# Kernel tuning notes

Measured on AMD Instinct MI355X. Metric: run time of the kernel, lower is better.

The kernel has to match this reference:

```python
import jax, jax.numpy as jnp
import numpy as np

N = 50000   # nodes
E = 800000  # edges (avg degree 16)
IN = 128
HID = 128
OUT = 64    # num classes


def setup_inputs() -> dict:
    key = jax.random.key(0)
    ks = jax.random.split(key, 10)
    x = jax.random.normal(ks[0], (N, IN), dtype=jnp.float32)
    edge_src = jax.random.randint(ks[1], (E,), 0, N)
    edge_dst = jax.random.randint(ks[2], (E,), 0, N)
    y = jax.random.randint(ks[3], (N,), 0, OUT)
    train_mask = jax.random.bernoulli(ks[4], 0.5, (N,))
    w = lambda k, sh: (jax.random.normal(k, sh, dtype=jnp.float32) * (1.0 / np.sqrt(sh[0]))).astype(jnp.float32)
    return dict(
        x=x, edge_src=edge_src, edge_dst=edge_dst, y=y, train_mask=train_mask,
        W1l=w(ks[5], (IN, HID)), b1=jnp.zeros((HID,), jnp.float32), W1r=w(ks[6], (IN, HID)),
        W2l=w(ks[7], (HID, OUT)), b2=jnp.zeros((OUT,), jnp.float32), W2r=w(ks[8], (HID, OUT)),
    )


def mean_aggr(h, src, dst, n):
    # sparse adjacency matmul with reduce='mean': for each dst node, mean of src features
    msg_sum = jax.ops.segment_sum(h[src], dst, num_segments=n)          # [N, D]
    cnt = jax.ops.segment_sum(jnp.ones((src.shape[0],), h.dtype), dst, num_segments=n)
    return msg_sum / jnp.maximum(cnt, 1.0)[:, None]


def reference(x, edge_src, edge_dst, y, train_mask, W1l, b1, W1r, W2l, b2, W2r):
    n = x.shape[0]
    # dropout(p=0.2, training=False) is identity in eval mode
    h = x
    # layer 1: SAGEConv = lin_l(mean_aggr(h)) + lin_r(h), then ReLU (+identity dropout)
    a = mean_aggr(h, edge_src, edge_dst, n)
    h = jax.nn.relu(a @ W1l + b1 + h @ W1r)
    # layer 2 (output layer)
    a = mean_aggr(h, edge_src, edge_dst, n)
    logits = a @ W2l + b2 + h @ W2r
    logp = jax.nn.log_softmax(logits, axis=1)
    # nll_loss over masked nodes (single chunk => loss / num_chunks with num_chunks=1)
    m = train_mask.astype(logp.dtype)
    nll = -jnp.take_along_axis(logp, y[:, None], axis=1)[:, 0]
    loss = jnp.sum(nll * m) / jnp.maximum(jnp.sum(m), 1.0)
    return loss
```

## Files before the change

kernel.cpp:

```cpp
#include <hip/hip_runtime.h>
#include <hip/hip_bf16.h>

typedef unsigned int uint;
typedef unsigned short u16;

#define DIN 128
#define DHID 128
#define DOUT 64
#define BSH 8
#define P3CHUNK 8192
#define P4MAX 6144

static inline size_t al256(size_t x) { return (x + 255) & ~(size_t)255; }

typedef __attribute__((ext_vector_type(8))) short short8;
typedef __attribute__((ext_vector_type(4))) float floatx4;
typedef __attribute__((ext_vector_type(2))) float floatx2;
typedef __attribute__((ext_vector_type(4))) int intx4;

__device__ inline float2 bf2x(uint v) {
    return make_float2(__uint_as_float(v << 16), __uint_as_float(v & 0xffff0000u));
}
__device__ inline uint packbf(float a, float b) {
    uint ua = __float_as_uint(a), ub = __float_as_uint(b);
    ua += 0x7fff + ((ua >> 16) & 1);
    ub += 0x7fff + ((ub >> 16) & 1);
    return (ua >> 16) | (ub & 0xffff0000u);
}
__device__ inline u16 pb(float a) {
    uint u = __float_as_uint(a);
    u += 0x7fff + ((u >> 16) & 1);
    return (u16)(u >> 16);
}

__device__ inline floatx2 f8lo(uint v) {
#if __has_builtin(__builtin_amdgcn_cvt_pk_f32_fp8)
    return __builtin_amdgcn_cvt_pk_f32_fp8((int)v, false);
#else
    uint b0 = v & 0xffu, b1 = (v >> 8) & 0xffu;
    floatx2 r;
    r.x = __uint_as_float(((b0 & 0x80u) << 24) | ((b0 & 0x7fu) << 20)) * 0x1p120f;
    r.y = __uint_as_float(((b1 & 0x80u) << 24) | ((b1 & 0x7fu) << 20)) * 0x1p120f;
    return r;
#endif
}
__device__ inline floatx2 f8hi(uint v) {
#if __has_builtin(__builtin_amdgcn_cvt_pk_f32_fp8)
    return __builtin_amdgcn_cvt_pk_f32_fp8((int)v, true);
#else
    uint b0 = (v >> 16) & 0xffu, b1 = (v >> 24) & 0xffu;
    floatx2 r;
    r.x = __uint_as_float(((b0 & 0x80u) << 24) | ((b0 & 0x7fu) << 20)) * 0x1p120f;
    r.y = __uint_as_float(((b1 & 0x80u) << 24) | ((b1 & 0x7fu) << 20)) * 0x1p120f;
    return r;
#endif
}
__device__ inline uint enc8(float f) {
    uint ub = __float_as_uint(f * 0x1p-120f);
    uint s = (ub >> 24) & 0x80u;
    uint mag = ub & 0x7fffffffu;
    mag += 0x7ffffu + ((mag >> 20) & 1u);
    uint r = mag >> 20;
    if (r > 0x7eu) r = 0x7eu;
    return r | s;
}
__device__ inline uint packf8x4(float a, float b, float c, float d) {
#if __has_builtin(__builtin_amdgcn_cvt_pk_fp8_f32)
    int p = __builtin_amdgcn_cvt_pk_fp8_f32(a, b, 0, false);
    p = __builtin_amdgcn_cvt_pk_fp8_f32(c, d, p, true);
    return (uint)p;
#else
    return enc8(a) | (enc8(b) << 8) | (enc8(c) << 16) | (enc8(d) << 24);
#endif
}

__global__ __launch_bounds__(256) void pack_detect_kernel(
    const float* __restrict__ W1l, const float* __restrict__ W1r,
    const float* __restrict__ W2l, const float* __restrict__ W2r,
    u16* __restrict__ Wp1, u16* __restrict__ Wp2,
    const int* __restrict__ tm, int n_int, int* __restrict__ gflags) {
    if (blockIdx.x < 192) {
        int id = blockIdx.x * 256 + threadIdx.x;
        if (id < 32768) {
            int frag = id >> 9, e = id & 511;
            int lane = e >> 3, j = e & 7;
            int kc = frag >> 4, tn = frag & 15;
            int k = kc * 32 + (lane >> 4) * 8 + j;
            int ncol = tn * 16 + (lane & 15);
            float v = (ncol < 128) ? W1l[k * 128 + ncol] : W1r[k * 128 + ncol - 128];
            Wp1[id] = pb(v);
        } else if (id < 49152) {
            int id2 = id - 32768;
            int frag = id2 >> 9, e = id2 & 511;
            int lane = e >> 3, j = e & 7;
            int kc = frag >> 3, tn = frag & 7;
            int k = kc * 32 + (lane >> 4) * 8 + j;
            int ncol = tn * 16 + (lane & 15);
            float v = (ncol < 64) ? W2l[k * 64 + ncol] : W2r[k * 64 + ncol - 64];
            Wp2[id2] = pb(v);
        }
    } else {
        int i = (blockIdx.x - 192) * 256 + threadIdx.x;
        bool hf = false, ho = false;
        for (; i < n_int; i += 64 * 256) {
            int v = tm[i];
            hf |= (v == 0x3F800000);
            ho |= (v != 0 && v != 1 && v != 0x3F800000);
        }
        if (__any(hf) && (threadIdx.x & 63) == 0) atomicOr(&gflags[0], 1);
        if (__any(ho) && (threadIdx.x & 63) == 0) atomicOr(&gflags[1], 1);
    }
}

__global__ __launch_bounds__(256) void bhist_kernel(const int* __restrict__ dst, int e, int nb,
                                                    uint* __restrict__ bcounts) {
    __shared__ uint lh[512];
    for (int i = threadIdx.x; i < 512; i += 256) lh[i] = 0;
    __syncthreads();
    int nquad = (e + 3) >> 2;
    for (int i = blockIdx.x * 256 + threadIdx.x; i < nquad; i += gridDim.x * 256) {
        int base = i * 4;
        if (base + 4 <= e) {
            intx4 d = __builtin_nontemporal_load((const intx4*)(dst + base));
            atomicAdd(&lh[d.x >> BSH], 1u);
            atomicAdd(&lh[d.y >> BSH], 1u);
            atomicAdd(&lh[d.z >> BSH], 1u);
            atomicAdd(&lh[d.w >> BSH], 1u);
        } else {
            for (int k = base; k < e; ++k) atomicAdd(&lh[dst[k] >> BSH], 1u);
        }
    }
    __syncthreads();
    for (int i = threadIdx.x; i < nb; i += 256) {
        uint c = lh[i];
        if (c) atomicAdd(&bcounts[i], c);
    }
}

__global__ __launch_bounds__(256) void bscan_kernel(const uint* __restrict__ bcounts, int nb, int e,
                                                    uint* __restrict__ bbase, uint* __restrict__ bcursor,
                                                    int* __restrict__ offsets, int n) {
    __shared__ uint pws[4];
    int t = threadIdx.x;
    uint v0 = (2 * t < nb) ? bcounts[2 * t] : 0u;
    uint v1 = (2 * t + 1 < nb) ? bcounts[2 * t + 1] : 0u;
    uint s = v0 + v1;
    int lane = t & 63, wv = t >> 6;
    uint incl = s;
    #pragma unroll
    for (int d = 1; d < 64; d <<= 1) {
        uint u = (uint)__shfl_up((int)incl, d, 64);
        if (lane >= d) incl += u;
    }
    if (lane == 63) pws[wv] = incl;
    __syncthreads();
    uint woff = 0;
    #pragma unroll
    for (int i = 0; i < 4; ++i) if (i < wv) woff += pws[i];
    uint excl = woff + incl - s;
    if (2 * t < nb) { bbase[2 * t] = excl; bcursor[2 * t] = excl; }
    if (2 * t + 1 < nb) { bbase[2 * t + 1] = excl + v0; bcursor[2 * t + 1] = excl + v0; }
    if (t == 0) {
        uint tot = pws[0] + pws[1] + pws[2] + pws[3];
        bbase[nb] = tot;
        offsets[n] = e;
    }
}

__global__ __launch_bounds__(256) void partition_kernel(const int* __restrict__ src,
                                                        const int* __restrict__ dst, int e, int nb,
                                                        uint* __restrict__ bcursor,
                                                        uint* __restrict__ pairs) {
    __shared__ uint lh[512], lexcl[512], lbase[512], lpos[512];
    __shared__ uint st[P3CHUNK];
    __shared__ uint pws[4];
    int t = threadIdx.x;
    int e0 = blockIdx.x * P3CHUNK;
    int ecnt = min(P3CHUNK, e - e0);
    for (int i = t; i < 512; i += 256) { lh[i] = 0; lpos[i] = 0; }
    __syncthreads();
    for (int i = t; i < ecnt; i += 256)
        atomicAdd(&lh[dst[e0 + i] >> BSH], 1u);
    __syncthreads();
    {
        uint v0 = lh[2 * t], v1 = lh[2 * t + 1];
        uint s = v0 + v1;
        int lane = t & 63, wv = t >> 6;
        uint incl = s;
        #pragma unroll
        for (int d = 1; d < 64; d <<= 1) {
            uint u = (uint)__shfl_up((int)incl, d, 64);
            if (lane >= d) incl += u;
        }
        if (lane == 63) pws[wv] = incl;
        __syncthreads();
        uint woff = 0;
        #pragma unroll
        for (int i = 0; i < 4; ++i) if (i < wv) woff += pws[i];
        uint excl = woff + incl - s;
        lexcl[2 * t] = excl;
        lexcl[2 * t + 1] = excl + v0;
    }
    __syncthreads();
    for (int b = t; b < nb; b += 256) {
        uint c = lh[b];
        lbase[b] = c ? atomicAdd(&bcursor[b], c) : 0u;
    }
    __syncthreads();
    for (int i = t; i < ecnt; i += 256) {
        int d = dst[e0 + i];
        int s = src[e0 + i];
        int b = d >> BSH;
        uint slot = lexcl[b] + atomicAdd(&lpos[b], 1u);
        st[slot] = ((uint)(d & ((1 << BSH) - 1)) << 16) | (uint)s;
    }
    __syncthreads();
    int wv = t >> 6, lane = t & 63;
    for (int b = wv; b < nb; b += 4) {
        uint c = lh[b];
        uint lsrc = lexcl[b], gdst = lbase[b];
        for (uint k = lane; k < c; k += 64)
            pairs[gdst + k] = st[lsrc + k];
    }
}

__global__ __launch_bounds__(256) void emit_kernel(const uint* __restrict__ pairs,
                                                   const uint* __restrict__ bbase, int n,
                                                   u16* __restrict__ csr, int* __restrict__ offsets) {
    __shared__ uint cnt[256], lex[256];
    __shared__ u16 ob[P4MAX];
    __shared__ uint pws[4];
    int b = blockIdx.x, t = threadIdx.x;
    uint seg0 = bbase[b];
    int len = (int)(bbase[b + 1] - seg0);
    int n0 = b << BSH;
    cnt[t] = 0;
    __syncthreads();
    for (int i = t; i < len; i += 256)
        atomicAdd(&cnt[pairs[seg0 + i] >> 16], 1u);
    __syncthreads();
    uint v = cnt[t];
    int lane = t & 63, wv = t >> 6;
    uint incl = v;
    #pragma unroll
    for (int d = 1; d < 64; d <<= 1) {
        uint u = (uint)__shfl_up((int)incl, d, 64);
        if (lane >= d) incl += u;
    }
    if (lane == 63) pws[wv] = incl;
    __syncthreads();
    uint woff = 0;
    #pragma unroll
    for (int i = 0; i < 4; ++i) if (i < wv) woff += pws[i];
    uint excl = woff + incl - v;
    lex[t] = excl;
    if (n0 + t < n) offsets[n0 + t] = (int)(seg0 + excl);
    __syncthreads();
    cnt[t] = 0;
    __syncthreads();
    for (int i = t; i < len; i += 256) {
        uint p = pairs[seg0 + i];
        uint loc = p >> 16;
        uint slot = lex[loc] + atomicAdd(&cnt[loc], 1u);
        if (slot < P4MAX) ob[slot] = (u16)(p & 0xffffu);
        else csr[seg0 + slot] = (u16)(p & 0xffffu);
    }
    __syncthreads();
    int lim = min(len, P4MAX);
    for (int i = t; i < lim; i += 256) csr[seg0 + i] = ob[i];
}

__global__ __launch_bounds__(256) void hist_kernel(const int* __restrict__ dst, int e,
                                                   int* __restrict__ counts) {
    int base = (blockIdx.x * 256 + threadIdx.x) * 4;
    if (base + 4 <= e) {
        intx4 d = __builtin_nontemporal_load((const intx4*)(dst + base));
        atomicAdd(&counts[d.x], 1);
        atomicAdd(&counts[d.y], 1);
        atomicAdd(&counts[d.z], 1);
        atomicAdd(&counts[d.w], 1);
    } else {
        for (int i = base; i < e; ++i) atomicAdd(&counts[dst[i]], 1);
    }
}

__global__ __launch_bounds__(256) void scan_partial_kernel(const int* __restrict__ counts, int n,
                                                           int* __restrict__ partials) {
    int t = threadIdx.x;
    int base = blockIdx.x * 1024 + t * 4;
    int s = 0;
    if (base + 3 < n) {
        int4 v = *(const int4*)&counts[base];
        s = v.x + v.y + v.z + v.w;
    } else {
        for (int i = 0; i < 4; ++i) if (base + i < n) s += counts[base + i];
    }
    #pragma unroll
    for (int d = 32; d; d >>= 1) s += __shfl_down(s, d, 64);
    __shared__ int wsum[4];
    if ((t & 63) == 0) wsum[t >> 6] = s;
    __syncthreads();
    if (t == 0) partials[blockIdx.x] = wsum[0] + wsum[1] + wsum[2] + wsum[3];
}

__global__ void scan_top_kernel(int* __restrict__ partials, int nparts, int* __restrict__ total_out) {
    int lane = threadIdx.x;
    int v = (lane < nparts) ? partials[lane] : 0;
    int incl = v;
    #pragma unroll
    for (int d = 1; d < 64; d <<= 1) {
        int u = __shfl_up(incl, d, 64);
        if (lane >= d) incl += u;
    }
    if (lane < nparts) partials[lane] = incl - v;
    if (lane == 63) *total_out = incl;
}

__global__ __launch_bounds__(256) void scan_final_kernel(const int* __restrict__ counts, int n,
                                                         const int* __restrict__ partials,
                                                         int* __restrict__ offsets,
                                                         int* __restrict__ cursor) {
    int t = threadIdx.x;
    int base = blockIdx.x * 1024 + t * 4;
    int v0 = 0, v1 = 0, v2 = 0, v3 = 0;
    if (base + 3 < n) {
        int4 q = *(const int4*)&counts[base];
        v0 = q.x; v1 = q.y; v2 = q.z; v3 = q.w;
    } else {
        if (base + 0 < n) v0 = counts[base + 0];
        if (base + 1 < n) v1 = counts[base + 1];
        if (base + 2 < n) v2 = counts[base + 2];
        if (base + 3 < n) v3 = counts[base + 3];
    }
    int s = v0 + v1 + v2 + v3;
    int lane = t & 63, wid = t >> 6;
    int incl = s;
    #pragma unroll
    for (int d = 1; d < 64; d <<= 1) {
        int u = __shfl_up(incl, d, 64);
        if (lane >= d) incl += u;
    }
    __shared__ int wsum[4];
    if (lane == 63) wsum[wid] = incl;
    __syncthreads();
    int woff = 0;
    #pragma unroll
    for (int i = 0; i < 4; ++i) if (i < wid) woff += wsum[i];
    int run = partials[blockIdx.x] + woff + incl - s;
    if (base + 0 < n) { offsets[base + 0] = run; cursor[base + 0] = run; run += v0; }
    if (base + 1 < n) { offsets[base + 1] = run; cursor[base + 1] = run; run += v1; }
    if (base + 2 < n) { offsets[base + 2] = run; cursor[base + 2] = run; run += v2; }
    if (base + 3 < n) { offsets[base + 3] = run; cursor[base + 3] = run; run += v3; }
}

__global__ __launch_bounds__(256) void scatter_kernel(const int* __restrict__ src,
                                                      const int* __restrict__ dst, int e,
                                                      int* __restrict__ cursor,
                                                      uint* __restrict__ csr_src) {
    int base = (blockIdx.x * 256 + threadIdx.x) * 4;
    if (base + 4 <= e) {
        intx4 s = __builtin_nontemporal_load((const intx4*)(src + base));
        intx4 d = __builtin_nontemporal_load((const intx4*)(dst + base));
        int p0 = atomicAdd(&cursor[d.x], 1);
        int p1 = atomicAdd(&cursor[d.y], 1);
        int p2 = atomicAdd(&cursor[d.z], 1);
        int p3 = atomicAdd(&cursor[d.w], 1);
        csr_src[p0] = (uint)s.x;
        csr_src[p1] = (uint)s.y;
        csr_src[p2] = (uint)s.z;
        csr_src[p3] = (uint)s.w;
    } else {
        for (int i = base; i < e; ++i) {
            int p = atomicAdd(&cursor[dst[i]], 1);
            csr_src[p] = (uint)src[i];
        }
    }
}

__global__ __launch_bounds__(256) void gemm1_mfma(
    const float* __restrict__ X, const u16* __restrict__ Wp1,
    const float* __restrict__ b1,
    uint* __restrict__ P1f8, uint* __restrict__ Q1u, int n) {
    __shared__ u16 ep[4][16][260];
    int t = threadIdx.x;
    int w = t >> 6, lane = t & 63;
    int q = lane >> 4, c = lane & 15;
    int m0 = blockIdx.x * 64 + w * 16;
    int me = min(m0 + c, n - 1);
    const float* xrow = X + (size_t)me * 128 + q * 8;
    const u16* wbase = Wp1 + lane * 8;

    floatx4 acc[16];
    #pragma unroll
    for (int i = 0; i < 16; ++i) acc[i] = (floatx4){0.f, 0.f, 0.f, 0.f};

    #pragma unroll
    for (int kc = 0; kc < 4; ++kc) {
        float4 x0 = *(const float4*)(xrow + kc * 32);
        float4 x1 = *(const float4*)(xrow + kc * 32 + 4);
        union { short8 s; uint4 u; } a;
        a.u.x = packbf(x0.x, x0.y); a.u.y = packbf(x0.z, x0.w);
        a.u.z = packbf(x1.x, x1.y); a.u.w = packbf(x1.z, x1.w);
        #pragma unroll
        for (int tn = 0; tn < 16; ++tn) {
            union { short8 s; uint4 u; } b;
            b.u = *(const uint4*)(wbase + (kc * 16 + tn) * 512);
            acc[tn] = __builtin_amdgcn_mfma_f32_16x16x32_bf16(a.s, b.s, acc[tn], 0, 0, 0);
        }
    }

    #pragma unroll
    for (int tn = 0; tn < 16; ++tn) {
        int col = tn * 16 + c;
        float badd = (tn >= 8) ? b1[col - 128] : 0.f;
        #pragma unroll
        for (int i = 0; i < 4; ++i)
            ep[w][q * 4 + i][col] = pb(acc[tn][i] + badd);
    }
    for (int r = 0; r < 16; ++r) {
        int grow = m0 + r;
        if (grow >= n) break;
        uint2 v = *(const uint2*)&ep[w][r][lane * 4];
        if (lane < 32) {
            float2 e0 = bf2x(v.x), e1 = bf2x(v.y);
            P1f8[(size_t)grow * 32 + lane] = packf8x4(e0.x, e0.y, e1.x, e1.y);
        } else {
            *(uint2*)&Q1u[(size_t)grow * 64 + 2 * (lane - 32)] = v;
        }
    }
}

template <typename IT>
__global__ __launch_bounds__(256) void aggr1_kernel(
    const uint* __restrict__ P1f8, const uint* __restrict__ Q1u,
    const int* __restrict__ offsets, const IT* __restrict__ csr,
    uint* __restrict__ h1u, int n) {
    int node = (int)((blockIdx.x * (size_t)blockDim.x + threadIdx.x) >> 6);
    int lane = threadIdx.x & 63;
    int l = lane & 31, hw = lane >> 5;
    if (node >= n) return;
    int beg = offsets[node], end = offsets[node + 1];
    float a0 = 0.f, a1 = 0.f, a2 = 0.f, a3 = 0.f;
    int i = beg + hw;
    for (; i + 2 < end; i += 4) {
        int s0 = csr[i], s1 = csr[i + 2];
        uint v0 = P1f8[(size_t)s0 * 32 + l];
        uint v1 = P1f8[(size_t)s1 * 32 + l];
        floatx2 u0 = f8lo(v0), w0 = f8hi(v0);
        floatx2 u1 = f8lo(v1), w1 = f8hi(v1);
        a0 += u0.x + u1.x; a1 += u0.y + u1.y;
        a2 += w0.x + w1.x; a3 += w0.y + w1.y;
    }
    for (; i < end; i += 2) {
        int s = csr[i];
        uint v = P1f8[(size_t)s * 32 + l];
        floatx2 u = f8lo(v), w2 = f8hi(v);
        a0 += u.x; a1 += u.y; a2 += w2.x; a3 += w2.y;
    }
    a0 += __shfl_xor(a0, 32, 64);
    a1 += __shfl_xor(a1, 32, 64);
    a2 += __shfl_xor(a2, 32, 64);
    a3 += __shfl_xor(a3, 32, 64);
    if (hw == 0) {
        float inv = 1.0f / (float)max(end - beg, 1);
        uint2 qv = *(const uint2*)&Q1u[(size_t)node * 64 + l * 2];
        float2 q0 = bf2x(qv.x), q1 = bf2x(qv.y);
        float r0 = fmaxf(fmaf(a0, inv, q0.x), 0.f);
        float r1 = fmaxf(fmaf(a1, inv, q0.y), 0.f);
        float r2 = fmaxf(fmaf(a2, inv, q1.x), 0.f);
        float r3 = fmaxf(fmaf(a3, inv, q1.y), 0.f);
        uint2 o;
        o.x = packbf(r0, r1);
        o.y = packbf(r2, r3);
        *(uint2*)&h1u[(size_t)node * 64 + l * 2] = o;
    }
}

__global__ __launch_bounds__(256) void gemm2_mfma(
    const uint* __restrict__ H1u, const u16* __restrict__ Wp2,
    const float* __restrict__ b2,
    uint* __restrict__ P2f8, uint* __restrict__ Q2u, int n) {
    __shared__ u16 ep[4][16][132];
    int t = threadIdx.x;
    int w = t >> 6, lane = t & 63;
    int q = lane >> 4, c = lane & 15;
    int m0 = blockIdx.x * 64 + w * 16;
    int me = min(m0 + c, n - 1);
    const u16* hrow = (const u16*)H1u + (size_t)me * 128 + q * 8;
    const u16* wbase = Wp2 + lane * 8;

    floatx4 acc[8];
    #pragma unroll
    for (int i = 0; i < 8; ++i) acc[i] = (floatx4){0.f, 0.f, 0.f, 0.f};

    #pragma unroll
    for (int kc = 0; kc < 4; ++kc) {
        union { short8 s; uint4 u; } a;
        a.u = *(const uint4*)(hrow + kc * 32);
        #pragma unroll
        for (int tn = 0; tn < 8; ++tn) {
            union { short8 s; uint4 u; } b;
            b.u = *(const uint4*)(wbase + (kc * 8 + tn) * 512);
            acc[tn] = __builtin_amdgcn_mfma_f32_16x16x32_bf16(a.s, b.s, acc[tn], 0, 0, 0);
        }
    }

    #pragma unroll
    for (int tn = 0; tn < 8; ++tn) {
        int col = tn * 16 + c;
        float badd = (tn >= 4) ? b2[col - 64] : 0.f;
        #pragma unroll
        for (int i = 0; i < 4; ++i)
            ep[w][q * 4 + i][col] = pb(acc[tn][i] + badd);
    }
    for (int r = 0; r < 16; ++r) {
        int grow = m0 + r;
        if (grow >= n) break;
        if (lane < 16) {
            uint2 v = *(const uint2*)&ep[w][r][lane * 4];
            float2 e0 = bf2x(v.x), e1 = bf2x(v.y);
            P2f8[(size_t)grow * 16 + lane] = packf8x4(e0.x, e0.y, e1.x, e1.y);
        } else if (lane < 48) {
            uint v = *(const uint*)&ep[w][r][64 + (lane - 16) * 2];
            Q2u[(size_t)grow * 32 + (lane - 16)] = v;
        }
    }
}

template <typename IT>
__global__ __launch_bounds__(1024) void loss_kernel(
    const uint* __restrict__ P2f8, const uint* __restrict__ Q2u,
    const int* __restrict__ offsets, const IT* __restrict__ csr,
    const int* __restrict__ y, const void* __restrict__ tmask,
    const int* __restrict__ gflags, float2* __restrict__ bpart, int n) {
    int wid = threadIdx.x >> 6;
    int node = blockIdx.x * 16 + wid;
    int lane = threadIdx.x & 63;
    int l = lane & 15, qw = lane >> 4;
    float num = 0.f, den = 0.f;
    if (node < n) {
        int beg = offsets[node], end = offsets[node + 1];
        float a0 = 0.f, a1 = 0.f, a2 = 0.f, a3 = 0.f;
        int i = beg + qw;
        for (; i + 4 < end; i += 8) {
            int s0 = csr[i], s1 = csr[i + 4];
            uint v0 = P2f8[(size_t)s0 * 16 + l];
            uint v1 = P2f8[(size_t)s1 * 16 + l];
            floatx2 u0 = f8lo(v0), w0 = f8hi(v0);
            floatx2 u1 = f8lo(v1), w1 = f8hi(v1);
            a0 += u0.x + u1.x; a1 += u0.y + u1.y;
            a2 += w0.x + w1.x; a3 += w0.y + w1.y;
        }
        for (; i < end; i += 4) {
            int s = csr[i];
            uint v = P2f8[(size_t)s * 16 + l];
            floatx2 u = f8lo(v), w2 = f8hi(v);
            a0 += u.x; a1 += u.y; a2 += w2.x; a3 += w2.y;
        }
        #pragma unroll
        for (int d = 16; d <= 32; d <<= 1) {
            a0 += __shfl_xor(a0, d, 64);
            a1 += __shfl_xor(a1, d, 64);
            a2 += __shfl_xor(a2, d, 64);
            a3 += __shfl_xor(a3, d, 64);
        }
        float inv = 1.0f / (float)max(end - beg, 1);
        uint2 qv = *(const uint2*)&Q2u[(size_t)node * 32 + l * 2];
        float2 q0 = bf2x(qv.x), q1 = bf2x(qv.y);
        float L0 = fmaf(a0, inv, q0.x);
        float L1 = fmaf(a1, inv, q0.y);
        float L2 = fmaf(a2, inv, q1.x);
        float L3 = fmaf(a3, inv, q1.y);
        float mx = fmaxf(fmaxf(L0, L1), fmaxf(L2, L3));
        #pragma unroll
        for (int d = 1; d <= 8; d <<= 1) mx = fmaxf(mx, __shfl_xor(mx, d, 64));
        float s = __expf(L0 - mx) + __expf(L1 - mx) + __expf(L2 - mx) + __expf(L3 - mx);
        #pragma unroll
        for (int d = 1; d <= 8; d <<= 1) s += __shfl_xor(s, d, 64);
        int cls = y[node];
        int srcl = (cls >> 2) & 15;
        float c0 = __shfl(L0, srcl, 64);
        float c1 = __shfl(L1, srcl, 64);
        float c2 = __shfl(L2, srcl, 64);
        float c3 = __shfl(L3, srcl, 64);
        int sel = cls & 3;
        float Lc = (sel == 0) ? c0 : (sel == 1) ? c1 : (sel == 2) ? c2 : c3;
        float logp = (Lc - mx) - __logf(s);
        int f = gflags[0] ? 2 : (gflags[1] ? 0 : 1);
        bool m;
        if (f == 0)      m = ((const unsigned char*)tmask)[node] != 0;
        else if (f == 1) m = ((const int*)tmask)[node] != 0;
        else             m = ((const float*)tmask)[node] != 0.f;
        if (m) { num = -logp; den = 1.f; }
    }
    __shared__ float2 wacc[16];
    if (lane == 0) wacc[wid] = make_float2(num, den);
    __syncthreads();
    if (threadIdx.x == 0) {
        float rx = 0.f, ry = 0.f;
        #pragma unroll
        for (int i = 0; i < 16; ++i) { rx += wacc[i].x; ry += wacc[i].y; }
        bpart[blockIdx.x] = make_float2(rx, ry);
    }
}

__global__ __launch_bounds__(1024) void finalize_kernel(const float2* __restrict__ bpart, int nb,
                                                        float* __restrict__ out) {
    int t = threadIdx.x;
    float sx = 0.f, sy = 0.f;
    for (int i = t; i < nb; i += 1024) { float2 v = bpart[i]; sx += v.x; sy += v.y; }
    #pragma unroll
    for (int d = 32; d; d >>= 1) { sx += __shfl_down(sx, d, 64); sy += __shfl_down(sy, d, 64); }
    __shared__ float2 wacc[16];
    if ((t & 63) == 0) wacc[t >> 6] = make_float2(sx, sy);
    __syncthreads();
    if (t == 0) {
        float nx = 0.f, ny = 0.f;
        #pragma unroll
        for (int i = 0; i < 16; ++i) { nx += wacc[i].x; ny += wacc[i].y; }
        out[0] = nx / fmaxf(ny, 1.f);
    }
}

extern "C" void kernel_launch(void* const* d_in, const int* in_sizes, int n_in,
                              void* d_out, int out_size, void* d_ws, size_t ws_size,
                              hipStream_t stream) {
    const float* x        = (const float*)d_in[0];
    const int*   edge_src = (const int*)d_in[1];
    const int*   edge_dst = (const int*)d_in[2];
    const int*   y        = (const int*)d_in[3];
    const void*  tmask    = (const void*)d_in[4];
    const float* W1l      = (const float*)d_in[5];
    const float* b1       = (const float*)d_in[6];
    const float* W1r      = (const float*)d_in[7];
    const float* W2l      = (const float*)d_in[8];
    const float* b2       = (const float*)d_in[9];
    const float* W2r      = (const float*)d_in[10];

    const int N = in_sizes[0] / DIN;
    const int E = in_sizes[1];
    const int nb_loss = (N + 15) / 16;
    const bool small_idx = (N <= 65535);
    const int nb = (N + 255) >> BSH;

    char* ws = (char*)d_ws;
    int* gflags = (int*)ws;
    size_t off = 256;
    int* offsets  = (int*)(ws + off); off += al256(((size_t)N + 1) * 4);
    uint* bcounts = (uint*)(ws + off); off += al256(513 * 4);
    uint* bbase   = (uint*)(ws + off); off += al256(513 * 4);
    uint* bcursor = (uint*)(ws + off); off += al256(513 * 4);
    uint* pairs   = (uint*)(ws + off); off += al256((size_t)E * 4);
    void* csr     = (void*)(ws + off); off += al256((size_t)E * 4);
    int* counts   = (int*)(ws + off); off += al256((size_t)N * 4);
    int* cursor   = (int*)(ws + off); off += al256((size_t)N * 4);
    int* spart    = (int*)(ws + off); off += al256(64 * 4);
    float2* bpart = (float2*)(ws + off); off += al256((size_t)nb_loss * 8);
    u16* Wp1      = (u16*)(ws + off); off += al256(32768 * 2);
    u16* Wp2      = (u16*)(ws + off); off += al256(16384 * 2);
    uint* P1f8    = (uint*)(ws + off); off += al256((size_t)N * 32 * 4);
    uint* h1u     = (uint*)(ws + off); off += al256((size_t)N * 64 * 4);
    uint* Q1u     = (uint*)(ws + off); off += al256((size_t)N * 64 * 4);
    uint* P2f8    = Q1u;
    uint* Q2u     = Q1u + (size_t)N * 16;

    hipMemsetAsync(ws, 0, 256, stream);

    pack_detect_kernel<<<256, 256, 0, stream>>>(W1l, W1r, W2l, W2r, Wp1, Wp2,
                                                (const int*)tmask, N / 4, gflags);

    if (small_idx) {
        hipMemsetAsync(bcounts, 0, 513 * 4, stream);
        bhist_kernel<<<256, 256, 0, stream>>>(edge_dst, E, nb, bcounts);
        bscan_kernel<<<1, 256, 0, stream>>>(bcounts, nb, E, bbase, bcursor, offsets, N);
        int pblocks = (E + P3CHUNK - 1) / P3CHUNK;
        partition_kernel<<<pblocks, 256, 0, stream>>>(edge_src, edge_dst, E, nb, bcursor, pairs);
        emit_kernel<<<nb, 256, 0, stream>>>(pairs, bbase, N, (u16*)csr, offsets);
    } else {
        hipMemsetAsync(counts, 0, (size_t)N * 4, stream);
        int eb4 = (E + 1023) / 1024;
        hist_kernel<<<eb4, 256, 0, stream>>>(edge_dst, E, counts);
        int sb = (N + 1023) / 1024;
        scan_partial_kernel<<<sb, 256, 0, stream>>>(counts, N, spart);
        scan_top_kernel<<<1, 64, 0, stream>>>(spart, sb, &offsets[N]);
        scan_final_kernel<<<sb, 256, 0, stream>>>(counts, N, spart, offsets, cursor);
        scatter_kernel<<<eb4, 256, 0, stream>>>(edge_src, edge_dst, E, cursor, (uint*)csr);
    }

    int gb = (N + 63) / 64;
    int ab = (N + 3) / 4;

    gemm1_mfma<<<gb, 256, 0, stream>>>(x, Wp1, b1, P1f8, Q1u, N);
    if (small_idx)
        aggr1_kernel<u16><<<ab, 256, 0, stream>>>(P1f8, Q1u, offsets, (const u16*)csr, h1u, N);
    else
        aggr1_kernel<uint><<<ab, 256, 0, stream>>>(P1f8, Q1u, offsets, (const uint*)csr, h1u, N);
    gemm2_mfma<<<gb, 256, 0, stream>>>(h1u, Wp2, b2, P2f8, Q2u, N);
    if (small_idx)
        loss_kernel<u16><<<nb_loss, 1024, 0, stream>>>(P2f8, Q2u, offsets, (const u16*)csr, y, tmask, gflags, bpart, N);
    else
        loss_kernel<uint><<<nb_loss, 1024, 0, stream>>>(P2f8, Q2u, offsets, (const uint*)csr, y, tmask, gflags, bpart, N);

    finalize_kernel<<<1, 1024, 0, stream>>>(bpart, nb_loss, (float*)d_out);
}
```

Baseline: 238.0 us.

## Fuse setup kernels, co-schedule emit with GEMM1, enlarge GEMM tiles, atomic loss finalize

Merges weight packing, mask detection and the bucket histogram into one launch, and runs the CSR emit blocks alongside the independent GEMM1 blocks in a single grid. Both GEMMs now compute 32 rows per wave instead of 16, reusing each loaded weight fragment twice. The gather loops in both aggregation passes are unrolled to four neighbors per iteration. The separate finalize kernel is replaced by atomic accumulation with a last-block ticket. This cuts launch count and idle gaps, at the cost of more registers per thread and float atomics whose summation order is nondeterministic.

Result: slower. 325.6 us (+36.8%).

```diff
diff --git a/kernel.cpp b/kernel.cpp
--- a/kernel.cpp
+++ b/kernel.cpp
@@ -74,16 +74,19 @@
 #endif
 }
 
-__global__ __launch_bounds__(256) void pack_detect_kernel(
+__global__ __launch_bounds__(256) void pack_detect_bhist_kernel(
     const float* __restrict__ W1l, const float* __restrict__ W1r,
     const float* __restrict__ W2l, const float* __restrict__ W2r,
     u16* __restrict__ Wp1, u16* __restrict__ Wp2,
-    const int* __restrict__ tm, int n_int, int* __restrict__ gflags) {
-    if (blockIdx.x < 192) {
-        int id = blockIdx.x * 256 + threadIdx.x;
+    const int* __restrict__ tm, int n_int, int* __restrict__ gflags,
+    const int* __restrict__ dst, int e, int nb, uint* __restrict__ bcounts) {
+    __shared__ uint lh[512];
+    int bx = blockIdx.x;
+    if (bx < 192) {
+        int id = bx * 256 + threadIdx.x;
         if (id < 32768) {
-            int frag = id >> 9, e = id & 511;
-            int lane = e >> 3, j = e & 7;
+            int frag = id >> 9, el = id & 511;
+            int lane = el >> 3, j = el & 7;
             int kc = frag >> 4, tn = frag & 15;
             int k = kc * 32 + (lane >> 4) * 8 + j;
             int ncol = tn * 16 + (lane & 15);
@@ -91,16 +94,16 @@
             Wp1[id] = pb(v);
         } else if (id < 49152) {
             int id2 = id - 32768;
-            int frag = id2 >> 9, e = id2 & 511;
-            int lane = e >> 3, j = e & 7;
+            int frag = id2 >> 9, el = id2 & 511;
+            int lane = el >> 3, j = el & 7;
             int kc = frag >> 3, tn = frag & 7;
             int k = kc * 32 + (lane >> 4) * 8 + j;
             int ncol = tn * 16 + (lane & 15);
             float v = (ncol < 64) ? W2l[k * 64 + ncol] : W2r[k * 64 + ncol - 64];
             Wp2[id2] = pb(v);
         }
-    } else {
-        int i = (blockIdx.x - 192) * 256 + threadIdx.x;
+    } else if (bx < 256) {
+        int i = (bx - 192) * 256 + threadIdx.x;
         bool hf = false, ho = false;
         for (; i < n_int; i += 64 * 256) {
             int v = tm[i];
@@ -109,31 +112,27 @@
         }
         if (__any(hf) && (threadIdx.x & 63) == 0) atomicOr(&gflags[0], 1);
         if (__any(ho) && (threadIdx.x & 63) == 0) atomicOr(&gflags[1], 1);
-    }
-}
-
-__global__ __launch_bounds__(256) void bhist_kernel(const int* __restrict__ dst, int e, int nb,
-                                                    uint* __restrict__ bcounts) {
-    __shared__ uint lh[512];
-    for (int i = threadIdx.x; i < 512; i += 256) lh[i] = 0;
-    __syncthreads();
-    int nquad = (e + 3) >> 2;
-    for (int i = blockIdx.x * 256 + threadIdx.x; i < nquad; i += gridDim.x * 256) {
-        int base = i * 4;
-        if (base + 4 <= e) {
-            intx4 d = __builtin_nontemporal_load((const intx4*)(dst + base));
-            atomicAdd(&lh[d.x >> BSH], 1u);
-            atomicAdd(&lh[d.y >> BSH], 1u);
-            atomicAdd(&lh[d.z >> BSH], 1u);
-            atomicAdd(&lh[d.w >> BSH], 1u);
-        } else {
-            for (int k = base; k < e; ++k) atomicAdd(&lh[dst[k] >> BSH], 1u);
-        }
-    }
-    __syncthreads();
-    for (int i = threadIdx.x; i < nb; i += 256) {
-        uint c = lh[i];
-        if (c) atomicAdd(&bcounts[i], c);
+    } else {
+        for (int i = threadIdx.x; i < 512; i += 256) lh[i] = 0;
+        __syncthreads();
+        int nquad = (e + 3) >> 2;
+        for (int i = (bx - 256) * 256 + threadIdx.x; i < nquad; i += 256 * 256) {
+            int base = i * 4;
+            if (base + 4 <= e) {
+                intx4 d = __builtin_nontemporal_load((const intx4*)(dst + base));
+                atomicAdd(&lh[d.x >> BSH], 1u);
+                atomicAdd(&lh[d.y >> BSH], 1u);
+                atomicAdd(&lh[d.z >> BSH], 1u);
+                atomicAdd(&lh[d.w >> BSH], 1u);
+            } else {
+                for (int k = base; k < e; ++k) atomicAdd(&lh[dst[k] >> BSH], 1u);
+            }
+        }
+        __syncthreads();
+        for (int i = threadIdx.x; i < nb; i += 256) {
+            uint c = lh[i];
+            if (c) atomicAdd(&bcounts[i], c);
+        }
     }
 }
 
@@ -224,50 +223,118 @@
     }
 }
 
-__global__ __launch_bounds__(256) void emit_kernel(const uint* __restrict__ pairs,
-                                                   const uint* __restrict__ bbase, int n,
-                                                   u16* __restrict__ csr, int* __restrict__ offsets) {
-    __shared__ uint cnt[256], lex[256];
-    __shared__ u16 ob[P4MAX];
-    __shared__ uint pws[4];
-    int b = blockIdx.x, t = threadIdx.x;
-    uint seg0 = bbase[b];
-    int len = (int)(bbase[b + 1] - seg0);
-    int n0 = b << BSH;
-    cnt[t] = 0;
-    __syncthreads();
-    for (int i = t; i < len; i += 256)
-        atomicAdd(&cnt[pairs[seg0 + i] >> 16], 1u);
-    __syncthreads();
-    uint v = cnt[t];
-    int lane = t & 63, wv = t >> 6;
-    uint incl = v;
-    #pragma unroll
-    for (int d = 1; d < 64; d <<= 1) {
-        uint u = (uint)__shfl_up((int)incl, d, 64);
-        if (lane >= d) incl += u;
-    }
-    if (lane == 63) pws[wv] = incl;
-    __syncthreads();
-    uint woff = 0;
-    #pragma unroll
-    for (int i = 0; i < 4; ++i) if (i < wv) woff += pws[i];
-    uint excl = woff + incl - v;
-    lex[t] = excl;
-    if (n0 + t < n) offsets[n0 + t] = (int)(seg0 + excl);
-    __syncthreads();
-    cnt[t] = 0;
-    __syncthreads();
-    for (int i = t; i < len; i += 256) {
-        uint p = pairs[seg0 + i];
-        uint loc = p >> 16;
-        uint slot = lex[loc] + atomicAdd(&cnt[loc], 1u);
-        if (slot < P4MAX) ob[slot] = (u16)(p & 0xffffu);
-        else csr[seg0 + slot] = (u16)(p & 0xffffu);
-    }
-    __syncthreads();
-    int lim = min(len, P4MAX);
-    for (int i = t; i < lim; i += 256) csr[seg0 + i] = ob[i];
+__global__ __launch_bounds__(256) void emit_gemm1_kernel(
+    const uint* __restrict__ pairs, const uint* __restrict__ bbase,
+    u16* __restrict__ csr, int* __restrict__ offsets, int nb_emit,
+    const float* __restrict__ X, const u16* __restrict__ Wp1,
+    const float* __restrict__ b1,
+    uint* __restrict__ P1f8, uint* __restrict__ Q1u, int n) {
+    __shared__ u16 smem[4][16][260];
+    int t = threadIdx.x;
+    if (blockIdx.x < nb_emit) {
+        uint* cnt = (uint*)&smem[0][0][0];
+        uint* lex = cnt + 256;
+        uint* pws = lex + 256;
+        u16* ob = (u16*)(pws + 8);
+        int b = blockIdx.x;
+        uint seg0 = bbase[b];
+        int len = (int)(bbase[b + 1] - seg0);
+        int n0 = b << BSH;
+        cnt[t] = 0;
+        __syncthreads();
+        for (int i = t; i < len; i += 256)
+            atomicAdd(&cnt[pairs[seg0 + i] >> 16], 1u);
+        __syncthreads();
+        uint v = cnt[t];
+        int lane = t & 63, wv = t >> 6;
+        uint incl = v;
+        #pragma unroll
+        for (int d = 1; d < 64; d <<= 1) {
+            uint u = (uint)__shfl_up((int)incl, d, 64);
+            if (lane >= d) incl += u;
+        }
+        if (lane == 63) pws[wv] = incl;
+        __syncthreads();
+        uint woff = 0;
+        #pragma unroll
+        for (int i = 0; i < 4; ++i) if (i < wv) woff += pws[i];
+        uint excl = woff + incl - v;
+        lex[t] = excl;
+        if (n0 + t < n) offsets[n0 + t] = (int)(seg0 + excl);
+        __syncthreads();
+        cnt[t] = 0;
+        __syncthreads();
+        for (int i = t; i < len; i += 256) {
+            uint p = pairs[seg0 + i];
+            uint loc = p >> 16;
+            uint slot = lex[loc] + atomicAdd(&cnt[loc], 1u);
+            if (slot < P4MAX) ob[slot] = (u16)(p & 0xffffu);
+            else csr[seg0 + slot] = (u16)(p & 0xffffu);
+        }
+        __syncthreads();
+        int lim = min(len, P4MAX);
+        for (int i = t; i < lim; i += 256) csr[seg0 + i] = ob[i];
+        return;
+    }
+    int bid = blockIdx.x - nb_emit;
+    int w = t >> 6, lane = t & 63;
+    int q = lane >> 4, c = lane & 15;
+    int m0 = bid * 128 + w * 32;
+    int meA = min(m0 + c, n - 1);
+    int meB = min(m0 + 16 + c, n - 1);
+    const float* xrowA = X + (size_t)meA * 128 + q * 8;
+    const float* xrowB = X + (size_t)meB * 128 + q * 8;
+    const u16* wbase = Wp1 + lane * 8;
+
+    floatx4 acc[2][16];
+    #pragma unroll
+    for (int h = 0; h < 2; ++h)
+        #pragma unroll
+        for (int i = 0; i < 16; ++i) acc[h][i] = (floatx4){0.f, 0.f, 0.f, 0.f};
+
+    #pragma unroll
+    for (int kc = 0; kc < 4; ++kc) {
+        float4 xa0 = *(const float4*)(xrowA + kc * 32);
+        float4 xa1 = *(const float4*)(xrowA + kc * 32 + 4);
+        float4 xb0 = *(const float4*)(xrowB + kc * 32);
+        float4 xb1 = *(const float4*)(xrowB + kc * 32 + 4);
+        union { short8 s; uint4 u; } a0, a1;
+        a0.u.x = packbf(xa0.x, xa0.y); a0.u.y = packbf(xa0.z, xa0.w);
+        a0.u.z = packbf(xa1.x, xa1.y); a0.u.w = packbf(xa1.z, xa1.w);
+        a1.u.x = packbf(xb0.x, xb0.y); a1.u.y = packbf(xb0.z, xb0.w);
+        a1.u.z = packbf(xb1.x, xb1.y); a1.u.w = packbf(xb1.z, xb1.w);
+        #pragma unroll
+        for (int tn = 0; tn < 16; ++tn) {
+            union { short8 s; uint4 u; } b;
+            b.u = *(const uint4*)(wbase + (kc * 16 + tn) * 512);
+            acc[0][tn] = __builtin_amdgcn_mfma_f32_16x16x32_bf16(a0.s, b.s, acc[0][tn], 0, 0, 0);
+            acc[1][tn] = __builtin_amdgcn_mfma_f32_16x16x32_bf16(a1.s, b.s, acc[1][tn], 0, 0, 0);
+        }
+    }
+
+    #pragma unroll
+    for (int h = 0; h < 2; ++h) {
+        #pragma unroll
+        for (int tn = 0; tn < 16; ++tn) {
+            int col = tn * 16 + c;
+            float badd = (tn >= 8) ? b1[col - 128] : 0.f;
+            #pragma unroll
+            for (int i = 0; i < 4; ++i)
+                smem[w][q * 4 + i][col] = pb(acc[h][tn][i] + badd);
+        }
+        int r0 = m0 + h * 16;
+        for (int r = 0; r < 16; ++r) {
+            int grow = r0 + r;
+            if (grow >= n) continue;
+            uint2 v = *(const uint2*)&smem[w][r][lane * 4];
+            if (lane < 32) {
+                float2 e0 = bf2x(v.x), e1 = bf2x(v.y);
+                P1f8[(size_t)grow * 32 + lane] = packf8x4(e0.x, e0.y, e1.x, e1.y);
+            } else {
+                *(uint2*)&Q1u[(size_t)grow * 64 + 2 * (lane - 32)] = v;
+            }
+        }
+    }
 }
 
 __global__ __launch_bounds__(256) void hist_kernel(const int* __restrict__ dst, int e,
@@ -377,59 +444,6 @@
     }
 }
 
-__global__ __launch_bounds__(256) void gemm1_mfma(
-    const float* __restrict__ X, const u16* __restrict__ Wp1,
-    const float* __restrict__ b1,
-    uint* __restrict__ P1f8, uint* __restrict__ Q1u, int n) {
-    __shared__ u16 ep[4][16][260];
-    int t = threadIdx.x;
-    int w = t >> 6, lane = t & 63;
-    int q = lane >> 4, c = lane & 15;
-    int m0 = blockIdx.x * 64 + w * 16;
-    int me = min(m0 + c, n - 1);
-    const float* xrow = X + (size_t)me * 128 + q * 8;
-    const u16* wbase = Wp1 + lane * 8;
-
-    floatx4 acc[16];
-    #pragma unroll
-    for (int i = 0; i < 16; ++i) acc[i] = (floatx4){0.f, 0.f, 0.f, 0.f};
-
-    #pragma unroll
-    for (int kc = 0; kc < 4; ++kc) {
-        float4 x0 = *(const float4*)(xrow + kc * 32);
-        float4 x1 = *(const float4*)(xrow + kc * 32 + 4);
-        union { short8 s; uint4 u; } a;
-        a.u.x = packbf(x0.x, x0.y); a.u.y = packbf(x0.z, x0.w);
-        a.u.z = packbf(x1.x, x1.y); a.u.w = packbf(x1.z, x1.w);
-        #pragma unroll
-        for (int tn = 0; tn < 16; ++tn) {
-            union { short8 s; uint4 u; } b;
-            b.u = *(const uint4*)(wbase + (kc * 16 + tn) * 512);
-            acc[tn] = __builtin_amdgcn_mfma_f32_16x16x32_bf16(a.s, b.s, acc[tn], 0, 0, 0);
-        }
-    }
-
-    #pragma unroll
-    for (int tn = 0; tn < 16; ++tn) {
-        int col = tn * 16 + c;
-        float badd = (tn >= 8) ? b1[col - 128] : 0.f;
-        #pragma unroll
-        for (int i = 0; i < 4; ++i)
-            ep[w][q * 4 + i][col] = pb(acc[tn][i] + badd);
-    }
-    for (int r = 0; r < 16; ++r) {
-        int grow = m0 + r;
-        if (grow >= n) break;
-        uint2 v = *(const uint2*)&ep[w][r][lane * 4];
-        if (lane < 32) {
-            float2 e0 = bf2x(v.x), e1 = bf2x(v.y);
-            P1f8[(size_t)grow * 32 + lane] = packf8x4(e0.x, e0.y, e1.x, e1.y);
-        } else {
-            *(uint2*)&Q1u[(size_t)grow * 64 + 2 * (lane - 32)] = v;
-        }
-    }
-}
-
 template <typename IT>
 __global__ __launch_bounds__(256) void aggr1_kernel(
     const uint* __restrict__ P1f8, const uint* __restrict__ Q1u,
@@ -442,14 +456,20 @@
     int beg = offsets[node], end = offsets[node + 1];
     float a0 = 0.f, a1 = 0.f, a2 = 0.f, a3 = 0.f;
     int i = beg + hw;
-    for (; i + 2 < end; i += 4) {
-        int s0 = csr[i], s1 = csr[i + 2];
+    for (; i + 6 < end; i += 8) {
+        int s0 = csr[i], s1 = csr[i + 2], s2 = csr[i + 4], s3 = csr[i + 6];
         uint v0 = P1f8[(size_t)s0 * 32 + l];
         uint v1 = P1f8[(size_t)s1 * 32 + l];
+        uint v2 = P1f8[(size_t)s2 * 32 + l];
+        uint v3 = P1f8[(size_t)s3 * 32 + l];
         floatx2 u0 = f8lo(v0), w0 = f8hi(v0);
         floatx2 u1 = f8lo(v1), w1 = f8hi(v1);
-        a0 += u0.x + u1.x; a1 += u0.y + u1.y;
-        a2 += w0.x + w1.x; a3 += w0.y + w1.y;
+        floatx2 u2 = f8lo(v2), w2 = f8hi(v2);
+        floatx2 u3 = f8lo(v3), w3 = f8hi(v3);
+        a0 += (u0.x + u1.x) + (u2.x + u3.x);
+        a1 += (u0.y + u1.y) + (u2.y + u3.y);
+        a2 += (w0.x + w1.x) + (w2.x + w3.x);
+        a3 += (w0.y + w1.y) + (w2.y + w3.y);
     }
     for (; i < end; i += 2) {
         int s = csr[i];
@@ -484,45 +504,55 @@
     int t = threadIdx.x;
     int w = t >> 6, lane = t & 63;
     int q = lane >> 4, c = lane & 15;
-    int m0 = blockIdx.x * 64 + w * 16;
-    int me = min(m0 + c, n - 1);
-    const u16* hrow = (const u16*)H1u + (size_t)me * 128 + q * 8;
+    int m0 = blockIdx.x * 128 + w * 32;
+    int meA = min(m0 + c, n - 1);
+    int meB = min(m0 + 16 + c, n - 1);
+    const u16* hrowA = (const u16*)H1u + (size_t)meA * 128 + q * 8;
+    const u16* hrowB = (const u16*)H1u + (size_t)meB * 128 + q * 8;
     const u16* wbase = Wp2 + lane * 8;
 
-    floatx4 acc[8];
-    #pragma unroll
-    for (int i = 0; i < 8; ++i) acc[i] = (floatx4){0.f, 0.f, 0.f, 0.f};
+    floatx4 acc[2][8];
+    #pragma unroll
+    for (int h = 0; h < 2; ++h)
+        #pragma unroll
+        for (int i = 0; i < 8; ++i) acc[h][i] = (floatx4){0.f, 0.f, 0.f, 0.f};
 
     #pragma unroll
     for (int kc = 0; kc < 4; ++kc) {
-        union { short8 s; uint4 u; } a;
-        a.u = *(const uint4*)(hrow + kc * 32);
+        union { short8 s; uint4 u; } a0, a1;
+        a0.u = *(const uint4*)(hrowA + kc * 32);
+        a1.u = *(const uint4*)(hrowB + kc * 32);
         #pragma unroll
         for (int tn = 0; tn < 8; ++tn) {
             union { short8 s; uint4 u; } b;
             b.u = *(const uint4*)(wbase + (kc * 8 + tn) * 512);
-            acc[tn] = __builtin_amdgcn_mfma_f32_16x16x32_bf16(a.s, b.s, acc[tn], 0, 0, 0);
-        }
-    }
-
-    #pragma unroll
-    for (int tn = 0; tn < 8; ++tn) {
-        int col = tn * 16 + c;
-        float badd = (tn >= 4) ? b2[col - 64] : 0.f;
-        #pragma unroll
-        for (int i = 0; i < 4; ++i)
-            ep[w][q * 4 + i][col] = pb(acc[tn][i] + badd);
-    }
-    for (int r = 0; r < 16; ++r) {
-        int grow = m0 + r;
-        if (grow >= n) break;
-        if (lane < 16) {
-            uint2 v = *(const uint2*)&ep[w][r][lane * 4];
-            float2 e0 = bf2x(v.x), e1 = bf2x(v.y);
-            P2f8[(size_t)grow * 16 + lane] = packf8x4(e0.x, e0.y, e1.x, e1.y);
-        } else if (lane < 48) {
-            uint v = *(const uint*)&ep[w][r][64 + (lane - 16) * 2];
-            Q2u[(size_t)grow * 32 + (lane - 16)] = v;
+            acc[0][tn] = __builtin_amdgcn_mfma_f32_16x16x32_bf16(a0.s, b.s, acc[0][tn], 0, 0, 0);
+            acc[1][tn] = __builtin_amdgcn_mfma_f32_16x16x32_bf16(a1.s, b.s, acc[1][tn], 0, 0, 0);
+        }
+    }
+
+    #pragma unroll
+    for (int h = 0; h < 2; ++h) {
+        #pragma unroll
+        for (int tn = 0; tn < 8; ++tn) {
+            int col = tn * 16 + c;
+            float badd = (tn >= 4) ? b2[col - 64] : 0.f;
+            #pragma unroll
+            for (int i = 0; i < 4; ++i)
+                ep[w][q * 4 + i][col] = pb(acc[h][tn][i] + badd);
+        }
+        int r0 = m0 + h * 16;
+        for (int r = 0; r < 16; ++r) {
+            int grow = r0 + r;
+            if (grow >= n) continue;
+            if (lane < 16) {
+                uint2 v = *(const uint2*)&ep[w][r][lane * 4];
+                float2 e0 = bf2x(v.x), e1 = bf2x(v.y);
+                P2f8[(size_t)grow * 16 + lane] = packf8x4(e0.x, e0.y, e1.x, e1.y);
+            } else if (lane < 48) {
+                uint v = *(const uint*)&ep[w][r][64 + (lane - 16) * 2];
+                Q2u[(size_t)grow * 32 + (lane - 16)] = v;
+            }
         }
     }
 }
@@ -532,7 +562,8 @@
     const uint* __restrict__ P2f8, const uint* __restrict__ Q2u,
     const int* __restrict__ offsets, const IT* __restrict__ csr,
     const int* __restrict__ y, const void* __restrict__ tmask,
-    const int* __restrict__ gflags, float2* __restrict__ bpart, int n) {
+    const int* __restrict__ gflags, float* __restrict__ accum, uint* __restrict__ acnt,
+    float* __restrict__ out, int n) {
     int wid = threadIdx.x >> 6;
     int node = blockIdx.x * 16 + wid;
     int lane = threadIdx.x & 63;
@@ -542,14 +573,20 @@
         int beg = offsets[node], end = offsets[node + 1];
         float a0 = 0.f, a1 = 0.f, a2 = 0.f, a3 = 0.f;
         int i = beg + qw;
-        for (; i + 4 < end; i += 8) {
-            int s0 = csr[i], s1 = csr[i + 4];
+        for (; i + 12 < end; i += 16) {
+            int s0 = csr[i], s1 = csr[i + 4], s2 = csr[i + 8], s3 = csr[i + 12];
             uint v0 = P2f8[(size_t)s0 * 16 + l];
             uint v1 = P2f8[(size_t)s1 * 16 + l];
+            uint v2 = P2f8[(size_t)s2 * 16 + l];
+            uint v3 = P2f8[(size_t)s3 * 16 + l];
             floatx2 u0 = f8lo(v0), w0 = f8hi(v0);
             floatx2 u1 = f8lo(v1), w1 = f8hi(v1);
-            a0 += u0.x + u1.x; a1 += u0.y + u1.y;
-            a2 += w0.x + w1.x; a3 += w0.y + w1.y;
+            floatx2 u2 = f8lo(v2), w2 = f8hi(v2);
+            floatx2 u3 = f8lo(v3), w3 = f8hi(v3);
+            a0 += (u0.x + u1.x) + (u2.x + u3.x);
+            a1 += (u0.y + u1.y) + (u2.y + u3.y);
+            a2 += (w0.x + w1.x) + (w2.x + w3.x);
+            a3 += (w0.y + w1.y) + (w2.y + w3.y);
         }
         for (; i < end; i += 4) {
             int s = csr[i];
@@ -600,25 +637,15 @@
         float rx = 0.f, ry = 0.f;
         #pragma unroll
         for (int i = 0; i < 16; ++i) { rx += wacc[i].x; ry += wacc[i].y; }
-        bpart[blockIdx.x] = make_float2(rx, ry);
-    }
-}
-
-__global__ __launch_bounds__(1024) void finalize_kernel(const float2* __restrict__ bpart, int nb,
-                                                        float* __restrict__ out) {
-    int t = threadIdx.x;
-    float sx = 0.f, sy = 0.f;
-    for (int i = t; i < nb; i += 1024) { float2 v = bpart[i]; sx += v.x; sy += v.y; }
-    #pragma unroll
-    for (int d = 32; d; d >>= 1) { sx += __shfl_down(sx, d, 64); sy += __shfl_down(sy, d, 64); }
-    __shared__ float2 wacc[16];
-    if ((t & 63) == 0) wacc[t >> 6] = make_float2(sx, sy);
-    __syncthreads();
-    if (t == 0) {
-        float nx = 0.f, ny = 0.f;
-        #pragma unroll
-        for (int i = 0; i < 16; ++i) { nx += wacc[i].x; ny += wacc[i].y; }
-        out[0] = nx / fmaxf(ny, 1.f);
+        atomicAdd(&accum[0], rx);
+        atomicAdd(&accum[1], ry);
+        __threadfence();
+        uint tick = atomicAdd(acnt, 1u);
+        if (tick == gridDim.x - 1) {
+            float nx = atomicAdd(&accum[0], 0.f);
+            float ny = atomicAdd(&accum[1], 0.f);
+            out[0] = nx / fmaxf(ny, 1.f);
+        }
     }
 }
 
@@ -644,18 +671,19 @@
     const int nb = (N + 255) >> BSH;
 
     char* ws = (char*)d_ws;
-    int* gflags = (int*)ws;
+    int* gflags  = (int*)ws;
+    float* accum = (float*)(ws + 16);
+    uint* acnt   = (uint*)(ws + 24);
     size_t off = 256;
-    int* offsets  = (int*)(ws + off); off += al256(((size_t)N + 1) * 4);
     uint* bcounts = (uint*)(ws + off); off += al256(513 * 4);
     uint* bbase   = (uint*)(ws + off); off += al256(513 * 4);
     uint* bcursor = (uint*)(ws + off); off += al256(513 * 4);
+    int* offsets  = (int*)(ws + off); off += al256(((size_t)N + 1) * 4);
     uint* pairs   = (uint*)(ws + off); off += al256((size_t)E * 4);
     void* csr     = (void*)(ws + off); off += al256((size_t)E * 4);
     int* counts   = (int*)(ws + off); off += al256((size_t)N * 4);
     int* cursor   = (int*)(ws + off); off += al256((size_t)N * 4);
     int* spart    = (int*)(ws + off); off += al256(64 * 4);
-    float2* bpart = (float2*)(ws + off); off += al256((size_t)nb_loss * 8);
     u16* Wp1      = (u16*)(ws + off); off += al256(32768 * 2);
     u16* Wp2      = (u16*)(ws + off); off += al256(16384 * 2);
     uint* P1f8    = (uint*)(ws + off); off += al256((size_t)N * 32 * 4);
@@ -664,19 +692,28 @@
     uint* P2f8    = Q1u;
     uint* Q2u     = Q1u + (size_t)N * 16;
 
-    hipMemsetAsync(ws, 0, 256, stream);
-
-    pack_detect_kernel<<<256, 256, 0, stream>>>(W1l, W1r, W2l, W2r, Wp1, Wp2,
-                                                (const int*)tmask, N / 4, gflags);
+    hipMemsetAsync(ws, 0, 8192, stream);
+
+    int gb32 = (N + 127) / 128;
 
     if (small_idx) {
-        hipMemsetAsync(bcounts, 0, 513 * 4, stream);
-        bhist_kernel<<<256, 256, 0, stream>>>(edge_dst, E, nb, bcounts);
+        pack_detect_bhist_kernel<<<512, 256, 0, stream>>>(
+            W1l, W1r, W2l, W2r, Wp1, Wp2, (const int*)tmask, N / 4, gflags,
+            edge_dst, E, nb, bcounts);
         bscan_kernel<<<1, 256, 0, stream>>>(bcounts, nb, E, bbase, bcursor, offsets, N);
         int pblocks = (E + P3CHUNK - 1) / P3CHUNK;
         partition_kernel<<<pblocks, 256, 0, stream>>>(edge_src, edge_dst, E, nb, bcursor, pairs);
-        emit_kernel<<<nb, 256, 0, stream>>>(pairs, bbase, N, (u16*)csr, offsets);
+        emit_gemm1_kernel<<<nb + gb32, 256, 0, stream>>>(
+            pairs, bbase, (u16*)csr, offsets, nb, x, Wp1, b1, P1f8, Q1u, N);
+        int ab = (N + 3) / 4;
+        aggr1_kernel<u16><<<ab, 256, 0, stream>>>(P1f8, Q1u, offsets, (const u16*)csr, h1u, N);
+        gemm2_mfma<<<gb32, 256, 0, stream>>>(h1u, Wp2, b2, P2f8, Q2u, N);
+        loss_kernel<u16><<<nb_loss, 1024, 0, stream>>>(
+            P2f8, Q2u, offsets, (const u16*)csr, y, tmask, gflags, accum, acnt, (float*)d_out, N);
     } else {
+        pack_detect_bhist_kernel<<<256, 256, 0, stream>>>(
+            W1l, W1r, W2l, W2r, Wp1, Wp2, (const int*)tmask, N / 4, gflags,
+            edge_dst, E, nb, bcounts);
         hipMemsetAsync(counts, 0, (size_t)N * 4, stream);
         int eb4 = (E + 1023) / 1024;
         hist_kernel<<<eb4, 256, 0, stream>>>(edge_dst, E, counts);
@@ -685,21 +722,12 @@
         scan_top_kernel<<<1, 64, 0, stream>>>(spart, sb, &offsets[N]);
         scan_final_kernel<<<sb, 256, 0, stream>>>(counts, N, spart, offsets, cursor);
         scatter_kernel<<<eb4, 256, 0, stream>>>(edge_src, edge_dst, E, cursor, (uint*)csr);
-    }
-
-    int gb = (N + 63) / 64;
-    int ab = (N + 3) / 4;
-
-    gemm1_mfma<<<gb, 256, 0, stream>>>(x, Wp1, b1, P1f8, Q1u, N);
-    if (small_idx)
-        aggr1_kernel<u16><<<ab, 256, 0, stream>>>(P1f8, Q1u, offsets, (const u16*)csr, h1u, N);
-    else
+        emit_gemm1_kernel<<<gb32, 256, 0, stream>>>(
+            pairs, bbase, (u16*)csr, offsets, 0, x, Wp1, b1, P1f8, Q1u, N);
+        int ab = (N + 3) / 4;
         aggr1_kernel<uint><<<ab, 256, 0, stream>>>(P1f8, Q1u, offsets, (const uint*)csr, h1u, N);
-    gemm2_mfma<<<gb, 256, 0, stream>>>(h1u, Wp2, b2, P2f8, Q2u, N);
-    if (small_idx)
-        loss_kernel<u16><<<nb_loss, 1024, 0, stream>>>(P2f8, Q2u, offsets, (const u16*)csr, y, tmask, gflags, bpart, N);
-    else
-        loss_kernel<uint><<<nb_loss, 1024, 0, stream>>>(P2f8, Q2u, offsets, (const uint*)csr, y, tmask, gflags, bpart, N);
-
-    finalize_kernel<<<1, 1024, 0, stream>>>(bpart, nb_loss, (float*)d_out);
-}
+        gemm2_mfma<<<gb32, 256, 0, stream>>>(h1u, Wp2, b2, P2f8, Q2u, N);
+        loss_kernel<uint><<<nb_loss, 1024, 0, stream>>>(
+            P2f8, Q2u, offsets, (const uint*)csr, y, tmask, gflags, accum, acnt, (float*)d_out, N);
+    }
+}
```
